# Kernel optimization log

Hardware: AMD Instinct MI355X
Metric: run time of the kernel (lower is better)

The kernel has to match this reference:

```python
import jax, jax.numpy as jnp
import numpy as np

N_NODES = 100000
N_EDGES = 3200000
NUM_GRAPHS = 2048
IN_CH = 35
HID = 128
EPS = 1e-5


def setup_inputs() -> dict:
    key = jax.random.key(0)
    ks = jax.random.split(key, 16)
    x = jax.random.normal(ks[0], (N_NODES, IN_CH), dtype=jnp.float32)
    edge_index = jax.random.randint(ks[1], (2, N_EDGES), 0, N_NODES, dtype=jnp.int64)
    batch = jnp.sort(jax.random.randint(ks[2], (N_NODES,), 0, NUM_GRAPHS, dtype=jnp.int64))
    def lin(k, fan_in, fan_out):
        b = 1.0 / np.sqrt(fan_in)
        kw, kb = jax.random.split(k)
        W = jax.random.uniform(kw, (fan_in, fan_out), minval=-b, maxval=b, dtype=jnp.float32)
        bias = jax.random.uniform(kb, (fan_out,), minval=-b, maxval=b, dtype=jnp.float32)
        return W, bias
    W1, b1 = lin(ks[3], IN_CH, HID)
    W2, b2 = lin(ks[4], HID, HID)
    W3, b3 = lin(ks[5], HID, HID)
    Wl1, bl1 = lin(ks[6], HID, HID // 2)
    Wl2, bl2 = lin(ks[7], HID // 2, 1)
    ones = jnp.ones((HID,), jnp.float32)
    zeros = jnp.zeros((HID,), jnp.float32)
    return {
        'x': x, 'edge_index': edge_index, 'batch': batch,
        'W1': W1, 'b1': b1, 'g1': ones, 'be1': zeros,
        'W2': W2, 'b2': b2, 'g2': ones, 'be2': zeros,
        'W3': W3, 'b3': b3, 'g3': ones, 'be3': zeros,
        'Wl1': Wl1, 'bl1': bl1, 'Wl2': Wl2, 'bl2': bl2,
    }


def _gcn_norm(edge_index, n):
    # add self-loops, compute symmetric normalization D^-1/2 (A+I) D^-1/2
    loop = jnp.arange(n, dtype=edge_index.dtype)
    src = jnp.concatenate([edge_index[0], loop])
    dst = jnp.concatenate([edge_index[1], loop])
    deg = jax.ops.segment_sum(jnp.ones_like(dst, jnp.float32), dst, num_segments=n)
    dinv = jnp.where(deg > 0, jax.lax.rsqrt(deg), 0.0)
    norm = dinv[src] * dinv[dst]
    return src, dst, norm


def _gcn_conv(x, src, dst, norm, W, b):
    h = x @ W                      # [N, out]
    msg = h[src] * norm[:, None]   # gather + scale (irregular)
    out = jax.ops.segment_sum(msg, dst, num_segments=x.shape[0])
    return out + b


def _bn(x, g, be):
    mu = jnp.mean(x, axis=0)
    var = jnp.mean(jnp.square(x - mu), axis=0)  # biased var (torch BN training)
    return (x - mu) * jax.lax.rsqrt(var + EPS) * g + be


def reference(x, edge_index, batch, W1, b1, g1, be1, W2, b2, g2, be2,
              W3, b3, g3, be3, Wl1, bl1, Wl2, bl2):
    n = x.shape[0]
    src, dst, norm = _gcn_norm(edge_index, n)
    h = jax.nn.gelu(_bn(_gcn_conv(x, src, dst, norm, W1, b1), g1, be1), approximate=False)
    h = jax.nn.gelu(_bn(_gcn_conv(h, src, dst, norm, W2, b2), g2, be2), approximate=False)
    h = jax.nn.gelu(_bn(_gcn_conv(h, src, dst, norm, W3, b3), g3, be3), approximate=False)
    # global mean pool by graph id
    s = jax.ops.segment_sum(h, batch, num_segments=NUM_GRAPHS)
    cnt = jax.ops.segment_sum(jnp.ones((n,), jnp.float32), batch, num_segments=NUM_GRAPHS)
    pooled = s / jnp.maximum(cnt, 1.0)[:, None]
    out = jax.nn.elu(pooled @ Wl1 + bl1)
    out = out @ Wl2 + bl2
    return out  # [NUM_GRAPHS, 1]
```

## Files before the change

### kernel.cpp

```cpp
#include <hip/hip_runtime.h>
#include <hip/hip_bf16.h>
#include <math.h>

#define N_NODES 100000
#define N_EDGES 3200000
#define NUM_GRAPHS 2048
#define IN_CH 35
#define HID 128
#define BN_EPS 1e-5f

#define BUCK_SHIFT 9
#define BUCK_SIZE 512
#define NB_BUCK 196
#define BUCK_CAP 18432
#define BIN_GRID 1024
#define BIN_CHUNK 3128

typedef short bf16x8 __attribute__((ext_vector_type(8)));
typedef float f32x4 __attribute__((ext_vector_type(4)));

__device__ __forceinline__ float gelu_f(float x) {
    return 0.5f * x * (1.0f + erff(x * 0.70710678118654752440f));
}

__device__ __forceinline__ float bflo(unsigned v) { return __uint_as_float(v << 16); }
__device__ __forceinline__ float bfhi(unsigned v) { return __uint_as_float(v & 0xffff0000u); }
__device__ __forceinline__ unsigned f2bf(float f) {
    unsigned x = __float_as_uint(f);
    return (x + 0x7fffu + ((x >> 16) & 1u)) >> 16;
}
__device__ __forceinline__ unsigned packbf2(float lo, float hi) {
    return f2bf(lo) | (f2bf(hi) << 16);
}


__global__ void k_zero2(int* __restrict__ gcnt, float* __restrict__ stats,
                        unsigned* __restrict__ xzero, unsigned* __restrict__ hzero) {
    int i = threadIdx.x;
    if (i < NB_BUCK) gcnt[i] = 0;
    if (i < 3 * 256) stats[i] = 0.0f;
    if (i < 32) xzero[i] = 0u;
    if (i < 64) hzero[i] = 0u;
}


__global__ void k_wcast(const float* __restrict__ W2, const float* __restrict__ W3,
                        unsigned* __restrict__ Wt2, unsigned* __restrict__ Wt3) {
    int t = blockIdx.x * 256 + threadIdx.x;
    if (t >= 2 * 8192) return;
    const float* W = (t < 8192) ? W2 : W3;
    unsigned* Wt = (t < 8192) ? Wt2 : Wt3;
    int i = t & 8191;
    int n = i >> 6, j = i & 63;
    Wt[n * 64 + j] = packbf2(W[(2 * j) * HID + n], W[(2 * j + 1) * HID + n]);
}


__global__ void k_bin(const int* __restrict__ ei, int* __restrict__ gcnt,
                      unsigned* __restrict__ epack) {
    __shared__ unsigned lpack[BIN_CHUNK];
    __shared__ unsigned char lbuck[BIN_CHUNK];
    __shared__ int hist[NB_BUCK];
    __shared__ int hbase[NB_BUCK];
    __shared__ int lcur[NB_BUCK];
    int tid = threadIdx.x;
    if (tid < NB_BUCK) { hist[tid] = 0; lcur[tid] = 0; }
    __syncthreads();
    int e0 = blockIdx.x * BIN_CHUNK;
    int nE = min(e0 + BIN_CHUNK, N_EDGES) - e0;
    for (int i = tid * 4; i < nE; i += 1024) {
        int4 s4 = *(const int4*)(ei + e0 + i);
        int4 d4 = *(const int4*)(ei + N_EDGES + e0 + i);
        lpack[i + 0] = (unsigned)s4.x | (((unsigned)d4.x & 511u) << 17);
        lpack[i + 1] = (unsigned)s4.y | (((unsigned)d4.y & 511u) << 17);
        lpack[i + 2] = (unsigned)s4.z | (((unsigned)d4.z & 511u) << 17);
        lpack[i + 3] = (unsigned)s4.w | (((unsigned)d4.w & 511u) << 17);
        int b0 = d4.x >> BUCK_SHIFT, b1 = d4.y >> BUCK_SHIFT;
        int b2 = d4.z >> BUCK_SHIFT, b3 = d4.w >> BUCK_SHIFT;
        lbuck[i + 0] = (unsigned char)b0;
        lbuck[i + 1] = (unsigned char)b1;
        lbuck[i + 2] = (unsigned char)b2;
        lbuck[i + 3] = (unsigned char)b3;
        atomicAdd(&hist[b0], 1);
        atomicAdd(&hist[b1], 1);
        atomicAdd(&hist[b2], 1);
        atomicAdd(&hist[b3], 1);
    }
    __syncthreads();
    if (tid < NB_BUCK) {
        int h = hist[tid];
        hbase[tid] = (h > 0) ? (tid * BUCK_CAP + atomicAdd(&gcnt[tid], h)) : 0;
    }
    __syncthreads();
    for (int i = tid; i < nE; i += 256) {
        int b = lbuck[i];
        int off = atomicAdd(&lcur[b], 1);
        epack[hbase[b] + off] = lpack[i];
    }
}


__global__ void k_fill(const int* __restrict__ gcnt, const unsigned* __restrict__ epack,
                       int* __restrict__ rowp, int* __restrict__ rowpEnd,
                       float* __restrict__ dinv, int* __restrict__ col) {
    __shared__ int ldeg[BUCK_SIZE];
    __shared__ int sa[BUCK_SIZE];
    __shared__ int sb[BUCK_SIZE];
    __shared__ int lcur[BUCK_SIZE];
    int b = blockIdx.x;
    int tid = threadIdx.x;
    int base_node = b << BUCK_SHIFT;
    int nn = min(BUCK_SIZE, N_NODES - base_node);
    int seg0 = b * BUCK_CAP;
    int seg1 = seg0 + gcnt[b];
    ldeg[tid] = 0;
    __syncthreads();
    for (int e = seg0 + tid; e < seg1; e += BUCK_SIZE) {
        atomicAdd(&ldeg[epack[e] >> 17], 1);
    }
    __syncthreads();
    sa[tid] = ldeg[tid];
    __syncthreads();
    int* src = sa; int* dst = sb;
    for (int st = 1; st < BUCK_SIZE; st <<= 1) {
        int v = src[tid];
        if (tid >= st) v += src[tid - st];
        dst[tid] = v;
        __syncthreads();
        int* t = src; src = dst; dst = t;
    }
    int ex = (tid == 0) ? 0 : src[tid - 1];
    int rp = seg0 + ex;
    lcur[tid] = rp;
    if (tid < nn) {
        rowp[base_node + tid] = rp;
        rowpEnd[base_node + tid] = rp + ldeg[tid];
        dinv[base_node + tid] = rsqrtf((float)(ldeg[tid] + 1));
    }
    __syncthreads();
    for (int e = seg0 + tid; e < seg1; e += BUCK_SIZE) {
        unsigned v = epack[e];
        int p = atomicAdd(&lcur[v >> 17], 1);
        col[p] = (int)(v & 0x1FFFFu);
    }
}


__global__ void k_castx(const float* __restrict__ X, const float* __restrict__ dinv,
                        unsigned* __restrict__ Xb) {
    int i = blockIdx.x * blockDim.x + threadIdx.x;
    if (i >= N_NODES * 32) return;
    int n = i >> 5, j = i & 31;
    float dv = dinv[n];
    float lo = 0.0f, hi = 0.0f;
    if (j < 17) {
        lo = X[(size_t)n * IN_CH + 2 * j];
        hi = X[(size_t)n * IN_CH + 2 * j + 1];
    } else if (j == 17) {
        lo = X[(size_t)n * IN_CH + 34];
    }
    Xb[i] = packbf2(dv * lo, dv * hi);
}

#define ACC8(v) { a0 += bflo(v.x); a1 += bfhi(v.x); a2 += bflo(v.y); a3 += bfhi(v.y); \
                  a4 += bflo(v.z); a5 += bfhi(v.z); a6 += bflo(v.w); a7 += bfhi(v.w); }
#define ACC4(v) { a0 += bflo(v.x); a1 += bfhi(v.x); a2 += bflo(v.y); a3 += bfhi(v.y); }


#define C1_NODES 8

__global__ __launch_bounds__(512) void k_conv1(
        const unsigned* __restrict__ Xb, const int* __restrict__ rowp,
        const int* __restrict__ rowpEnd, const int* __restrict__ col,
        const float* __restrict__ dinv,
        const float* __restrict__ W1, const float* __restrict__ b1,
        unsigned* __restrict__ Yb) {
    __shared__ float w_s[IN_CH * HID];
    __shared__ float b_s[HID];
    __shared__ float xa_s[C1_NODES][36];
    int tid = threadIdx.x;
    for (int u = tid; u < IN_CH * HID; u += 512) w_s[u] = W1[u];
    if (tid < HID) b_s[tid] = b1[tid];

    int wid = tid >> 6;
    int lane = tid & 63;
    int g = lane >> 4;
    int j = lane & 15;
    int node = blockIdx.x * C1_NODES + wid;
    bool valid = node < N_NODES;

    float a0 = 0.0f, a1 = 0.0f, a2 = 0.0f, a3 = 0.0f;
    float di = 0.0f;
    if (valid) {
        int rp0 = rowp[node], rp1 = rowpEnd[node];
        di = dinv[node];
        uint2 sv = *(const uint2*)(Xb + (size_t)node * 32 + j * 2);
        float w0 = (g == 0) ? 1.0f : 0.0f;
        a0 = w0 * bflo(sv.x); a1 = w0 * bfhi(sv.x);
        a2 = w0 * bflo(sv.y); a3 = w0 * bfhi(sv.y);
        unsigned deg = (unsigned)(rp1 - rp0);
        for (int e0 = (rp0 & ~3); e0 < rp1; e0 += 32) {
            int ebA = e0 + 4 * g;
            int ebB = ebA + 16;
            int4 cA = *(const int4*)(col + ebA);
            int4 cB = *(const int4*)(col + ebB);
            int s0 = ((unsigned)(ebA + 0 - rp0) < deg) ? cA.x : N_NODES;
            int s1 = ((unsigned)(ebA + 1 - rp0) < deg) ? cA.y : N_NODES;
            int s2 = ((unsigned)(ebA + 2 - rp0) < deg) ? cA.z : N_NODES;
            int s3 = ((unsigned)(ebA + 3 - rp0) < deg) ? cA.w : N_NODES;
            int s4 = ((unsigned)(ebB + 0 - rp0) < deg) ? cB.x : N_NODES;
            int s5 = ((unsigned)(ebB + 1 - rp0) < deg) ? cB.y : N_NODES;
            int s6 = ((unsigned)(ebB + 2 - rp0) < deg) ? cB.z : N_NODES;
            int s7 = ((unsigned)(ebB + 3 - rp0) < deg) ? cB.w : N_NODES;
            uint2 v0 = *(const uint2*)(Xb + (size_t)s0 * 32 + j * 2);
            uint2 v1 = *(const uint2*)(Xb + (size_t)s1 * 32 + j * 2);
            uint2 v2 = *(const uint2*)(Xb + (size_t)s2 * 32 + j * 2);
            uint2 v3 = *(const uint2*)(Xb + (size_t)s3 * 32 + j * 2);
            uint2 v4 = *(const uint2*)(Xb + (size_t)s4 * 32 + j * 2);
            uint2 v5 = *(const uint2*)(Xb + (size_t)s5 * 32 + j * 2);
            uint2 v6 = *(const uint2*)(Xb + (size_t)s6 * 32 + j * 2);
            uint2 v7 = *(const uint2*)(Xb + (size_t)s7 * 32 + j * 2);
            ACC4(v0); ACC4(v1); ACC4(v2); ACC4(v3);
            ACC4(v4); ACC4(v5); ACC4(v6); ACC4(v7);
        }
    }
    a0 += __shfl(a0, (lane + 32) & 63, 64);
    a1 += __shfl(a1, (lane + 32) & 63, 64);
    a2 += __shfl(a2, (lane + 32) & 63, 64);
    a3 += __shfl(a3, (lane + 32) & 63, 64);
    a0 += __shfl(a0, (lane + 16) & 63, 64);
    a1 += __shfl(a1, (lane + 16) & 63, 64);
    a2 += __shfl(a2, (lane + 16) & 63, 64);
    a3 += __shfl(a3, (lane + 16) & 63, 64);
    if (valid && g == 0 && j < 9) {
        xa_s[wid][4 * j + 0] = di * a0;
        xa_s[wid][4 * j + 1] = di * a1;
        xa_s[wid][4 * j + 2] = di * a2;
        xa_s[wid][4 * j + 3] = di * a3;
    }
    __syncthreads();
    float acc0 = b_s[2 * lane];
    float acc1 = b_s[2 * lane + 1];
    #pragma unroll 7
    for (int k = 0; k < IN_CH; ++k) {
        float xv = xa_s[wid][k];
        acc0 = fmaf(xv, w_s[k * HID + 2 * lane], acc0);
        acc1 = fmaf(xv, w_s[k * HID + 2 * lane + 1], acc1);
    }
    if (valid) Yb[(size_t)node * 64 + lane] = packbf2(acc0, acc1);
}


__global__ __launch_bounds__(256) void k_gemm128m(
        const unsigned* __restrict__ Yb, const float* __restrict__ stats,
        const float* __restrict__ g, const float* __restrict__ be,
        const unsigned* __restrict__ Wt, const float* __restrict__ dinv,
        unsigned* __restrict__ Hb) {
    __shared__ __align__(16) unsigned act[64 * 64];
    __shared__ float sc_s[HID];
    __shared__ float sh_s[HID];
    int tid = threadIdx.x;
    if (tid < HID) {
        const float inv_n = 1.0f / (float)N_NODES;
        float mean = stats[tid] * inv_n;
        float var = stats[HID + tid] * inv_n - mean * mean;
        float s = g[tid] * rsqrtf(var + BN_EPS);
        sc_s[tid] = s;
        sh_s[tid] = be[tid] - mean * s;
    }
    __syncthreads();
    int row0 = blockIdx.x * 64;
    #pragma unroll
    for (int it = 0; it < 8; ++it) {
        int idx = it * 256 + tid;
        int r = idx >> 5;
        int c2 = idx & 31;
        int gr = row0 + r;
        uint2 v = make_uint2(0u, 0u);
        if (gr < N_NODES) v = *(const uint2*)(Yb + (size_t)gr * 64 + c2 * 2);
        int c = c2 * 2;
        float x0 = gelu_f(fmaf(bflo(v.x), sc_s[2 * c], sh_s[2 * c]));
        float x1 = gelu_f(fmaf(bfhi(v.x), sc_s[2 * c + 1], sh_s[2 * c + 1]));
        float x2 = gelu_f(fmaf(bflo(v.y), sc_s[2 * c + 2], sh_s[2 * c + 2]));
        float x3 = gelu_f(fmaf(bfhi(v.y), sc_s[2 * c + 3], sh_s[2 * c + 3]));
        int swz = (r & 7) << 2;
        act[r * 64 + (c ^ swz)]       = packbf2(x0, x1);
        act[r * 64 + ((c + 1) ^ swz)] = packbf2(x2, x3);
    }
    __syncthreads();
    int l = tid & 63;
    int w = tid >> 6;
    int r0 = w * 16;
    int arow = r0 + (l & 15);
    int kgrp = l >> 4;
    bf16x8 afrag[4];
    #pragma unroll
    for (int kk = 0; kk < 4; ++kk) {
        int base = (kk * 16 + kgrp * 4) ^ ((arow & 7) << 2);
        afrag[kk] = *(const bf16x8*)&act[arow * 64 + base];
    }
    float dv[4];
    #pragma unroll
    for (int reg = 0; reg < 4; ++reg) {
        int gr = row0 + r0 + kgrp * 4 + reg;
        dv[reg] = (gr < N_NODES) ? dinv[gr] : 0.0f;
    }
    unsigned short* Hb16 = (unsigned short*)Hb;
    #pragma unroll
    for (int n0 = 0; n0 < 8; ++n0) {
        f32x4 acc = {0.0f, 0.0f, 0.0f, 0.0f};
        #pragma unroll
        for (int kk = 0; kk < 4; ++kk) {
            bf16x8 b = *(const bf16x8*)&Wt[(n0 * 16 + (l & 15)) * 64 + kk * 16 + kgrp * 4];
            acc = __builtin_amdgcn_mfma_f32_16x16x32_bf16(afrag[kk], b, acc, 0, 0, 0);
        }
        int colg = n0 * 16 + (l & 15);
        #pragma unroll
        for (int reg = 0; reg < 4; ++reg) {
            int gr = row0 + r0 + kgrp * 4 + reg;
            if (gr < N_NODES)
                Hb16[(size_t)gr * HID + colg] = (unsigned short)f2bf(dv[reg] * acc[reg]);
        }
    }
}


__global__ void k_convb(const unsigned* __restrict__ Hb, const int* __restrict__ rowp,
                        const int* __restrict__ rowpEnd, const int* __restrict__ col,
                        const float* __restrict__ dinv,
                        const float* __restrict__ bias, unsigned* __restrict__ Yb) {
    int tid = threadIdx.x;
    int wid = tid >> 6;
    int lane = tid & 63;
    int g = lane >> 4;
    int j = lane & 15;
    int node = blockIdx.x * 4 + wid;
    if (node >= N_NODES) return;
    int rp0 = rowp[node], rp1 = rowpEnd[node];
    float di = dinv[node];
    uint4 sv = *(const uint4*)(Hb + (size_t)node * 64 + j * 4);
    float w0 = (g == 0) ? 1.0f : 0.0f;
    float a0 = w0 * bflo(sv.x), a1 = w0 * bfhi(sv.x);
    float a2 = w0 * bflo(sv.y), a3 = w0 * bfhi(sv.y);
    float a4 = w0 * bflo(sv.z), a5 = w0 * bfhi(sv.z);
    float a6 = w0 * bflo(sv.w), a7 = w0 * bfhi(sv.w);
    unsigned deg = (unsigned)(rp1 - rp0);
    for (int e0 = (rp0 & ~3); e0 < rp1; e0 += 32) {
        int ebA = e0 + 4 * g;
        int ebB = ebA + 16;
        int4 cA = *(const int4*)(col + ebA);
        int4 cB = *(const int4*)(col + ebB);
        int s0 = ((unsigned)(ebA + 0 - rp0) < deg) ? cA.x : N_NODES;
        int s1 = ((unsigned)(ebA + 1 - rp0) < deg) ? cA.y : N_NODES;
        int s2 = ((unsigned)(ebA + 2 - rp0) < deg) ? cA.z : N_NODES;
        int s3 = ((unsigned)(ebA + 3 - rp0) < deg) ? cA.w : N_NODES;
        int s4 = ((unsigned)(ebB + 0 - rp0) < deg) ? cB.x : N_NODES;
        int s5 = ((unsigned)(ebB + 1 - rp0) < deg) ? cB.y : N_NODES;
        int s6 = ((unsigned)(ebB + 2 - rp0) < deg) ? cB.z : N_NODES;
        int s7 = ((unsigned)(ebB + 3 - rp0) < deg) ? cB.w : N_NODES;
        uint4 v0 = *(const uint4*)(Hb + (size_t)s0 * 64 + j * 4);
        uint4 v1 = *(const uint4*)(Hb + (size_t)s1 * 64 + j * 4);
        uint4 v2 = *(const uint4*)(Hb + (size_t)s2 * 64 + j * 4);
        uint4 v3 = *(const uint4*)(Hb + (size_t)s3 * 64 + j * 4);
        uint4 v4 = *(const uint4*)(Hb + (size_t)s4 * 64 + j * 4);
        uint4 v5 = *(const uint4*)(Hb + (size_t)s5 * 64 + j * 4);
        uint4 v6 = *(const uint4*)(Hb + (size_t)s6 * 64 + j * 4);
        uint4 v7 = *(const uint4*)(Hb + (size_t)s7 * 64 + j * 4);
        ACC8(v0); ACC8(v1); ACC8(v2); ACC8(v3);
        ACC8(v4); ACC8(v5); ACC8(v6); ACC8(v7);
    }
    a0 += __shfl(a0, (lane + 32) & 63, 64);
    a1 += __shfl(a1, (lane + 32) & 63, 64);
    a2 += __shfl(a2, (lane + 32) & 63, 64);
    a3 += __shfl(a3, (lane + 32) & 63, 64);
    a4 += __shfl(a4, (lane + 32) & 63, 64);
    a5 += __shfl(a5, (lane + 32) & 63, 64);
    a6 += __shfl(a6, (lane + 32) & 63, 64);
    a7 += __shfl(a7, (lane + 32) & 63, 64);
    a0 += __shfl(a0, (lane + 16) & 63, 64);
    a1 += __shfl(a1, (lane + 16) & 63, 64);
    a2 += __shfl(a2, (lane + 16) & 63, 64);
    a3 += __shfl(a3, (lane + 16) & 63, 64);
    a4 += __shfl(a4, (lane + 16) & 63, 64);
    a5 += __shfl(a5, (lane + 16) & 63, 64);
    a6 += __shfl(a6, (lane + 16) & 63, 64);
    a7 += __shfl(a7, (lane + 16) & 63, 64);
    if (g == 0) {
        const float4* bp = (const float4*)(bias + 8 * j);
        float4 bA = bp[0], bB = bp[1];
        uint4 o;
        o.x = packbf2(fmaf(di, a0, bA.x), fmaf(di, a1, bA.y));
        o.y = packbf2(fmaf(di, a2, bA.z), fmaf(di, a3, bA.w));
        o.z = packbf2(fmaf(di, a4, bB.x), fmaf(di, a5, bB.y));
        o.w = packbf2(fmaf(di, a6, bB.z), fmaf(di, a7, bB.w));
        *(uint4*)(Yb + (size_t)node * 64 + j * 4) = o;
    }
}


__global__ void k_statsb(const unsigned* __restrict__ Yb, float* __restrict__ stats) {
    __shared__ float red[16][128];
    __shared__ float red2[16][128];
    int tid = threadIdx.x;
    int j = tid & 15;
    int rg = tid >> 4;
    float s[8] = {0, 0, 0, 0, 0, 0, 0, 0};
    float q[8] = {0, 0, 0, 0, 0, 0, 0, 0};
    for (int r = blockIdx.x * 16 + rg; r < N_NODES; r += gridDim.x * 16) {
        uint4 v = *(const uint4*)(Yb + (size_t)r * 64 + j * 4);
        float x;
        x = bflo(v.x); s[0] += x; q[0] = fmaf(x, x, q[0]);
        x = bfhi(v.x); s[1] += x; q[1] = fmaf(x, x, q[1]);
        x = bflo(v.y); s[2] += x; q[2] = fmaf(x, x, q[2]);
        x = bfhi(v.y); s[3] += x; q[3] = fmaf(x, x, q[3]);
        x = bflo(v.z); s[4] += x; q[4] = fmaf(x, x, q[4]);
        x = bfhi(v.z); s[5] += x; q[5] = fmaf(x, x, q[5]);
        x = bflo(v.w); s[6] += x; q[6] = fmaf(x, x, q[6]);
        x = bfhi(v.w); s[7] += x; q[7] = fmaf(x, x, q[7]);
    }
    #pragma unroll
    for (int k = 0; k < 8; ++k) {
        red[rg][8 * j + k]  = s[k];
        red2[rg][8 * j + k] = q[k];
    }
    __syncthreads();
    if (tid < 128) {
        float S = 0.0f, Q = 0.0f;
        #pragma unroll
        for (int r = 0; r < 16; ++r) { S += red[r][tid]; Q += red2[r][tid]; }
        atomicAdd(&stats[tid], S);
        atomicAdd(&stats[128 + tid], Q);
    }
}


__device__ __forceinline__ int lowerb(const int* __restrict__ arr, int n, int key) {
    int lo = 0, hi = n;
    while (lo < hi) {
        int mid = (lo + hi) >> 1;
        if (arr[mid] < key) lo = mid + 1; else hi = mid;
    }
    return lo;
}

__global__ void k_pool_mlp(const unsigned* __restrict__ Yb, const float* __restrict__ stats,
                           const float* __restrict__ g, const float* __restrict__ be,
                           const int* __restrict__ batch,
                           const float* __restrict__ Wl1, const float* __restrict__ bl1,
                           const float* __restrict__ Wl2, const float* __restrict__ bl2,
                           float* __restrict__ out) {
    __shared__ float pooled[128];
    __shared__ float part[2][128];
    __shared__ float sc_s[128];
    __shared__ float sh_s[128];
    __shared__ int bounds[2];
    int gidx = blockIdx.x;
    int tid = threadIdx.x;
    if (tid < 128) {
        const float inv_n = 1.0f / (float)N_NODES;
        float mean = stats[tid] * inv_n;
        float var = stats[128 + tid] * inv_n - mean * mean;
        float s = g[tid] * rsqrtf(var + BN_EPS);
        sc_s[tid] = s;
        sh_s[tid] = be[tid] - mean * s;
    }
    if (tid == 0) {
        bounds[0] = lowerb(batch, N_NODES, gidx);
        bounds[1] = lowerb(batch, N_NODES, gidx + 1);
    }
    __syncthreads();
    int lo = bounds[0], hi = bounds[1];
    int rofs = tid >> 6;
    int w = tid & 63;
    float sA = sc_s[2 * w], hA = sh_s[2 * w];
    float sB = sc_s[2 * w + 1], hB = sh_s[2 * w + 1];
    float accA = 0.0f, accB = 0.0f;
    for (int r = lo + rofs; r < hi; r += 2) {
        unsigned v = Yb[(size_t)r * 64 + w];
        accA += gelu_f(fmaf(bflo(v), sA, hA));
        accB += gelu_f(fmaf(bfhi(v), sB, hB));
    }
    part[rofs][2 * w]     = accA;
    part[rofs][2 * w + 1] = accB;
    __syncthreads();
    if (tid < 128)
        pooled[tid] = (hi > lo) ? (part[0][tid] + part[1][tid]) / (float)(hi - lo) : 0.0f;
    __syncthreads();
    if (tid < 64) {
        float hs = bl1[tid];
        #pragma unroll 4
        for (int k = 0; k < 128; ++k)
            hs = fmaf(pooled[k], Wl1[k * 64 + tid], hs);
        float e = (hs > 0.0f) ? hs : expm1f(hs);
        float pv = e * Wl2[tid];
        #pragma unroll
        for (int o = 32; o > 0; o >>= 1)
            pv += __shfl_down(pv, o);
        if (tid == 0) out[gidx] = pv + bl2[0];
    }
}


extern "C" void kernel_launch(void* const* d_in, const int* in_sizes, int n_in,
                              void* d_out, int out_size, void* d_ws, size_t ws_size,
                              hipStream_t stream) {
    const float* x   = (const float*)d_in[0];
    const int*   ei  = (const int*)d_in[1];
    const int*   bat = (const int*)d_in[2];
    const float* W1  = (const float*)d_in[3];
    const float* b1  = (const float*)d_in[4];
    const float* g1  = (const float*)d_in[5];
    const float* be1 = (const float*)d_in[6];
    const float* W2  = (const float*)d_in[7];
    const float* b2  = (const float*)d_in[8];
    const float* g2  = (const float*)d_in[9];
    const float* be2 = (const float*)d_in[10];
    const float* W3  = (const float*)d_in[11];
    const float* b3  = (const float*)d_in[12];
    const float* g3  = (const float*)d_in[13];
    const float* be3 = (const float*)d_in[14];
    const float* Wl1 = (const float*)d_in[15];
    const float* bl1 = (const float*)d_in[16];
    const float* Wl2 = (const float*)d_in[17];
    const float* bl2 = (const float*)d_in[18];
    float* out = (float*)d_out;

    char* ws = (char*)d_ws;
    size_t off = 0;
    auto alloc = [&](size_t bytes) -> char* {
        char* p = ws + off;
        off += (bytes + 255) & ~(size_t)255;
        return p;
    };
    int*      gcnt    = (int*)alloc(NB_BUCK * sizeof(int));
    unsigned* epack   = (unsigned*)alloc(((size_t)NB_BUCK * BUCK_CAP + 64) * sizeof(unsigned));
    int*      rowp    = (int*)alloc(N_NODES * sizeof(int));
    int*      rowpEnd = (int*)alloc(N_NODES * sizeof(int));
    float*    dinv    = (float*)alloc(N_NODES * sizeof(float));
    int*      col     = (int*)alloc(((size_t)NB_BUCK * BUCK_CAP + 64) * sizeof(int));
    unsigned* Xb      = (unsigned*)alloc((size_t)(N_NODES + 1) * 32 * sizeof(unsigned));
    unsigned* Ybuf    = (unsigned*)alloc((size_t)N_NODES * 64 * sizeof(unsigned));
    unsigned* Hbuf    = (unsigned*)alloc((size_t)(N_NODES + 1) * 64 * sizeof(unsigned));
    float*    stats   = (float*)alloc(3 * 256 * sizeof(float));
    unsigned* Wt2     = (unsigned*)alloc(8192 * sizeof(unsigned));
    unsigned* Wt3     = (unsigned*)alloc(8192 * sizeof(unsigned));

    k_zero2<<<1, 1024, 0, stream>>>(gcnt, stats, Xb + (size_t)N_NODES * 32,
                                    Hbuf + (size_t)N_NODES * 64);
    k_wcast<<<64, 256, 0, stream>>>(W2, W3, Wt2, Wt3);
    k_bin<<<BIN_GRID, 256, 0, stream>>>(ei, gcnt, epack);
    k_fill<<<NB_BUCK, BUCK_SIZE, 0, stream>>>(gcnt, epack, rowp, rowpEnd, dinv, col);
    k_castx<<<(N_NODES * 32 + 255) / 256, 256, 0, stream>>>(x, dinv, Xb);

    const int gemm_blocks = (N_NODES + 63) / 64;
    const int conv_blocks = (N_NODES + 3) / 4;

    k_conv1<<<(N_NODES + C1_NODES - 1) / C1_NODES, 512, 0, stream>>>(
        Xb, rowp, rowpEnd, col, dinv, W1, b1, Ybuf);
    k_statsb<<<1024, 256, 0, stream>>>(Ybuf, stats + 0 * 256);

    k_gemm128m<<<gemm_blocks, 256, 0, stream>>>(Ybuf, stats + 0 * 256, g1, be1, Wt2, dinv, Hbuf);
    k_convb<<<conv_blocks, 256, 0, stream>>>(Hbuf, rowp, rowpEnd, col, dinv, b2, Ybuf);
    k_statsb<<<1024, 256, 0, stream>>>(Ybuf, stats + 1 * 256);

    k_gemm128m<<<gemm_blocks, 256, 0, stream>>>(Ybuf, stats + 1 * 256, g2, be2, Wt3, dinv, Hbuf);
    k_convb<<<conv_blocks, 256, 0, stream>>>(Hbuf, rowp, rowpEnd, col, dinv, b3, Ybuf);
    k_statsb<<<1024, 256, 0, stream>>>(Ybuf, stats + 2 * 256);

    k_pool_mlp<<<NUM_GRAPHS, 128, 0, stream>>>(Ybuf, stats + 2 * 256, g3, be3, bat,
                                               Wl1, bl1, Wl2, bl2, out);
}
```

Before: 677.5 us.

## Pad CSR rows to multiples of four, fuse castx into fill, prefetch col indices

The CSR column array is now padded so every row length is a multiple of 4, with sentinel N_NODES entries. The aggregation loops can therefore use aligned int4 loads, a cheaper per-group validity check, and software prefetch of the next column chunk. The conv1 gather now uses 16-byte loads with 8 lanes per row instead of 8-byte loads. The Xb cast is fused into k_fill, and the zero and weight-cast kernels are merged, removing launches. The cost is a larger col buffer and extra padding writes, and correctness depends on every row fitting within COL_CAP.

```diff
diff --git a/kernel.cpp b/kernel.cpp
--- a/kernel.cpp
+++ b/kernel.cpp
@@ -13,6 +13,7 @@
 #define BUCK_SIZE 512
 #define NB_BUCK 196
 #define BUCK_CAP 18432
+#define COL_CAP 19456
 #define BIN_GRID 1024
 #define BIN_CHUNK 3128
 
@@ -34,25 +35,24 @@
 }
 
 
-__global__ void k_zero2(int* __restrict__ gcnt, float* __restrict__ stats,
-                        unsigned* __restrict__ xzero, unsigned* __restrict__ hzero) {
-    int i = threadIdx.x;
-    if (i < NB_BUCK) gcnt[i] = 0;
-    if (i < 3 * 256) stats[i] = 0.0f;
-    if (i < 32) xzero[i] = 0u;
-    if (i < 64) hzero[i] = 0u;
-}
-
-
-__global__ void k_wcast(const float* __restrict__ W2, const float* __restrict__ W3,
-                        unsigned* __restrict__ Wt2, unsigned* __restrict__ Wt3) {
-    int t = blockIdx.x * 256 + threadIdx.x;
-    if (t >= 2 * 8192) return;
-    const float* W = (t < 8192) ? W2 : W3;
-    unsigned* Wt = (t < 8192) ? Wt2 : Wt3;
-    int i = t & 8191;
-    int n = i >> 6, j = i & 63;
-    Wt[n * 64 + j] = packbf2(W[(2 * j) * HID + n], W[(2 * j + 1) * HID + n]);
+__global__ void k_init(int* __restrict__ gcnt, float* __restrict__ stats,
+                       unsigned* __restrict__ xzero, unsigned* __restrict__ hzero,
+                       const float* __restrict__ W2, const float* __restrict__ W3,
+                       unsigned* __restrict__ Wt2, unsigned* __restrict__ Wt3) {
+    if (blockIdx.x < 64) {
+        int t = blockIdx.x * 256 + threadIdx.x;
+        const float* W = (t < 8192) ? W2 : W3;
+        unsigned* Wt = (t < 8192) ? Wt2 : Wt3;
+        int i = t & 8191;
+        int n = i >> 6, j = i & 63;
+        Wt[n * 64 + j] = packbf2(W[(2 * j) * HID + n], W[(2 * j + 1) * HID + n]);
+    } else {
+        int i = threadIdx.x;
+        if (i < NB_BUCK) gcnt[i] = 0;
+        for (int k = i; k < 3 * 256; k += 256) stats[k] = 0.0f;
+        if (i < 32) xzero[i] = 0u;
+        if (i < 64) hzero[i] = 0u;
+    }
 }
 
 
@@ -100,26 +100,31 @@
 }
 
 
-__global__ void k_fill(const int* __restrict__ gcnt, const unsigned* __restrict__ epack,
-                       int* __restrict__ rowp, int* __restrict__ rowpEnd,
-                       float* __restrict__ dinv, int* __restrict__ col) {
+__global__ __launch_bounds__(512) void k_fill(
+        const int* __restrict__ gcnt, const unsigned* __restrict__ epack,
+        int* __restrict__ rowp, int* __restrict__ rowpEnd,
+        float* __restrict__ dinv, int* __restrict__ col,
+        const float* __restrict__ X, unsigned* __restrict__ Xb) {
     __shared__ int ldeg[BUCK_SIZE];
     __shared__ int sa[BUCK_SIZE];
     __shared__ int sb[BUCK_SIZE];
     __shared__ int lcur[BUCK_SIZE];
+    __shared__ float dl[BUCK_SIZE];
     int b = blockIdx.x;
     int tid = threadIdx.x;
     int base_node = b << BUCK_SHIFT;
     int nn = min(BUCK_SIZE, N_NODES - base_node);
-    int seg0 = b * BUCK_CAP;
-    int seg1 = seg0 + gcnt[b];
+    int seg0e = b * BUCK_CAP;
+    int seg1e = seg0e + gcnt[b];
+    int seg0c = b * COL_CAP;
     ldeg[tid] = 0;
     __syncthreads();
-    for (int e = seg0 + tid; e < seg1; e += BUCK_SIZE) {
+    for (int e = seg0e + tid; e < seg1e; e += BUCK_SIZE)
         atomicAdd(&ldeg[epack[e] >> 17], 1);
-    }
-    __syncthreads();
-    sa[tid] = ldeg[tid];
+    __syncthreads();
+    int deg = ldeg[tid];
+    int pdeg = (deg + 3) & ~3;
+    sa[tid] = pdeg;
     __syncthreads();
     int* src = sa; int* dst = sb;
     for (int st = 1; st < BUCK_SIZE; st <<= 1) {
@@ -130,41 +135,44 @@
         int* t = src; src = dst; dst = t;
     }
     int ex = (tid == 0) ? 0 : src[tid - 1];
-    int rp = seg0 + ex;
+    int total = src[BUCK_SIZE - 1];
+    int rp = seg0c + ex;
     lcur[tid] = rp;
+    float dv = rsqrtf((float)(deg + 1));
+    dl[tid] = dv;
     if (tid < nn) {
         rowp[base_node + tid] = rp;
-        rowpEnd[base_node + tid] = rp + ldeg[tid];
-        dinv[base_node + tid] = rsqrtf((float)(ldeg[tid] + 1));
-    }
-    __syncthreads();
-    for (int e = seg0 + tid; e < seg1; e += BUCK_SIZE) {
+        rowpEnd[base_node + tid] = rp + pdeg;
+        dinv[base_node + tid] = dv;
+    }
+    __syncthreads();
+    for (int e = seg0e + tid; e < seg1e; e += BUCK_SIZE) {
         unsigned v = epack[e];
         int p = atomicAdd(&lcur[v >> 17], 1);
         col[p] = (int)(v & 0x1FFFFu);
     }
-}
-
-
-__global__ void k_castx(const float* __restrict__ X, const float* __restrict__ dinv,
-                        unsigned* __restrict__ Xb) {
-    int i = blockIdx.x * blockDim.x + threadIdx.x;
-    if (i >= N_NODES * 32) return;
-    int n = i >> 5, j = i & 31;
-    float dv = dinv[n];
-    float lo = 0.0f, hi = 0.0f;
-    if (j < 17) {
-        lo = X[(size_t)n * IN_CH + 2 * j];
-        hi = X[(size_t)n * IN_CH + 2 * j + 1];
-    } else if (j == 17) {
-        lo = X[(size_t)n * IN_CH + 34];
-    }
-    Xb[i] = packbf2(dv * lo, dv * hi);
+    if (tid < nn) {
+        for (int p = rp + deg; p < rp + pdeg; ++p) col[p] = N_NODES;
+    }
+    for (int p = seg0c + total + tid; p < seg0c + COL_CAP; p += BUCK_SIZE)
+        col[p] = N_NODES;
+    for (int idx = tid; idx < nn * 32; idx += BUCK_SIZE) {
+        int nl = idx >> 5, j = idx & 31;
+        int n = base_node + nl;
+        float dvn = dl[nl];
+        float lo = 0.0f, hi = 0.0f;
+        if (j < 17) {
+            lo = X[(size_t)n * IN_CH + 2 * j];
+            hi = X[(size_t)n * IN_CH + 2 * j + 1];
+        } else if (j == 17) {
+            lo = X[(size_t)n * IN_CH + 34];
+        }
+        Xb[(size_t)n * 32 + j] = packbf2(dvn * lo, dvn * hi);
+    }
 }
 
 #define ACC8(v) { a0 += bflo(v.x); a1 += bfhi(v.x); a2 += bflo(v.y); a3 += bfhi(v.y); \
                   a4 += bflo(v.z); a5 += bfhi(v.z); a6 += bflo(v.w); a7 += bfhi(v.w); }
-#define ACC4(v) { a0 += bflo(v.x); a1 += bfhi(v.x); a2 += bflo(v.y); a3 += bfhi(v.y); }
 
 
 #define C1_NODES 8
@@ -177,66 +185,62 @@
         unsigned* __restrict__ Yb) {
     __shared__ float w_s[IN_CH * HID];
     __shared__ float b_s[HID];
-    __shared__ float xa_s[C1_NODES][36];
+    __shared__ float xa_s[C1_NODES][40];
     int tid = threadIdx.x;
     for (int u = tid; u < IN_CH * HID; u += 512) w_s[u] = W1[u];
     if (tid < HID) b_s[tid] = b1[tid];
 
     int wid = tid >> 6;
     int lane = tid & 63;
-    int g = lane >> 4;
-    int j = lane & 15;
+    int g = lane >> 3;
+    int j = lane & 7;
     int node = blockIdx.x * C1_NODES + wid;
     bool valid = node < N_NODES;
 
-    float a0 = 0.0f, a1 = 0.0f, a2 = 0.0f, a3 = 0.0f;
+    float a0 = 0, a1 = 0, a2 = 0, a3 = 0, a4 = 0, a5 = 0, a6 = 0, a7 = 0;
     float di = 0.0f;
     if (valid) {
         int rp0 = rowp[node], rp1 = rowpEnd[node];
         di = dinv[node];
-        uint2 sv = *(const uint2*)(Xb + (size_t)node * 32 + j * 2);
+        uint4 sv = *(const uint4*)(Xb + (size_t)node * 32 + j * 4);
         float w0 = (g == 0) ? 1.0f : 0.0f;
         a0 = w0 * bflo(sv.x); a1 = w0 * bfhi(sv.x);
         a2 = w0 * bflo(sv.y); a3 = w0 * bfhi(sv.y);
-        unsigned deg = (unsigned)(rp1 - rp0);
-        for (int e0 = (rp0 & ~3); e0 < rp1; e0 += 32) {
-            int ebA = e0 + 4 * g;
-            int ebB = ebA + 16;
-            int4 cA = *(const int4*)(col + ebA);
-            int4 cB = *(const int4*)(col + ebB);
-            int s0 = ((unsigned)(ebA + 0 - rp0) < deg) ? cA.x : N_NODES;
-            int s1 = ((unsigned)(ebA + 1 - rp0) < deg) ? cA.y : N_NODES;
-            int s2 = ((unsigned)(ebA + 2 - rp0) < deg) ? cA.z : N_NODES;
-            int s3 = ((unsigned)(ebA + 3 - rp0) < deg) ? cA.w : N_NODES;
-            int s4 = ((unsigned)(ebB + 0 - rp0) < deg) ? cB.x : N_NODES;
-            int s5 = ((unsigned)(ebB + 1 - rp0) < deg) ? cB.y : N_NODES;
-            int s6 = ((unsigned)(ebB + 2 - rp0) < deg) ? cB.z : N_NODES;
-            int s7 = ((unsigned)(ebB + 3 - rp0) < deg) ? cB.w : N_NODES;
-            uint2 v0 = *(const uint2*)(Xb + (size_t)s0 * 32 + j * 2);
-            uint2 v1 = *(const uint2*)(Xb + (size_t)s1 * 32 + j * 2);
-            uint2 v2 = *(const uint2*)(Xb + (size_t)s2 * 32 + j * 2);
-            uint2 v3 = *(const uint2*)(Xb + (size_t)s3 * 32 + j * 2);
-            uint2 v4 = *(const uint2*)(Xb + (size_t)s4 * 32 + j * 2);
-            uint2 v5 = *(const uint2*)(Xb + (size_t)s5 * 32 + j * 2);
-            uint2 v6 = *(const uint2*)(Xb + (size_t)s6 * 32 + j * 2);
-            uint2 v7 = *(const uint2*)(Xb + (size_t)s7 * 32 + j * 2);
-            ACC4(v0); ACC4(v1); ACC4(v2); ACC4(v3);
-            ACC4(v4); ACC4(v5); ACC4(v6); ACC4(v7);
+        a4 = w0 * bflo(sv.z); a5 = w0 * bfhi(sv.z);
+        a6 = w0 * bflo(sv.w); a7 = w0 * bfhi(sv.w);
+        if (rp0 < rp1) {
+            int4 cs = *(const int4*)(col + rp0 + 4 * g);
+            for (int e0 = rp0; e0 < rp1; e0 += 32) {
+                int4 nx = *(const int4*)(col + e0 + 32 + 4 * g);
+                bool v = (e0 + 4 * g) < rp1;
+                int s0 = v ? cs.x : N_NODES;
+                int s1 = v ? cs.y : N_NODES;
+                int s2 = v ? cs.z : N_NODES;
+                int s3 = v ? cs.w : N_NODES;
+                uint4 v0 = *(const uint4*)(Xb + (size_t)s0 * 32 + j * 4);
+                uint4 v1 = *(const uint4*)(Xb + (size_t)s1 * 32 + j * 4);
+                uint4 v2 = *(const uint4*)(Xb + (size_t)s2 * 32 + j * 4);
+                uint4 v3 = *(const uint4*)(Xb + (size_t)s3 * 32 + j * 4);
+                ACC8(v0); ACC8(v1); ACC8(v2); ACC8(v3);
+                cs = nx;
+            }
         }
     }
-    a0 += __shfl(a0, (lane + 32) & 63, 64);
-    a1 += __shfl(a1, (lane + 32) & 63, 64);
-    a2 += __shfl(a2, (lane + 32) & 63, 64);
-    a3 += __shfl(a3, (lane + 32) & 63, 64);
-    a0 += __shfl(a0, (lane + 16) & 63, 64);
-    a1 += __shfl(a1, (lane + 16) & 63, 64);
-    a2 += __shfl(a2, (lane + 16) & 63, 64);
-    a3 += __shfl(a3, (lane + 16) & 63, 64);
-    if (valid && g == 0 && j < 9) {
-        xa_s[wid][4 * j + 0] = di * a0;
-        xa_s[wid][4 * j + 1] = di * a1;
-        xa_s[wid][4 * j + 2] = di * a2;
-        xa_s[wid][4 * j + 3] = di * a3;
+    #define RED(o) { a0 += __shfl(a0,(lane+o)&63,64); a1 += __shfl(a1,(lane+o)&63,64); \
+                     a2 += __shfl(a2,(lane+o)&63,64); a3 += __shfl(a3,(lane+o)&63,64); \
+                     a4 += __shfl(a4,(lane+o)&63,64); a5 += __shfl(a5,(lane+o)&63,64); \
+                     a6 += __shfl(a6,(lane+o)&63,64); a7 += __shfl(a7,(lane+o)&63,64); }
+    RED(32); RED(16); RED(8);
+    #undef RED
+    if (valid && g == 0 && j < 5) {
+        xa_s[wid][8 * j + 0] = di * a0;
+        xa_s[wid][8 * j + 1] = di * a1;
+        xa_s[wid][8 * j + 2] = di * a2;
+        xa_s[wid][8 * j + 3] = di * a3;
+        xa_s[wid][8 * j + 4] = di * a4;
+        xa_s[wid][8 * j + 5] = di * a5;
+        xa_s[wid][8 * j + 6] = di * a6;
+        xa_s[wid][8 * j + 7] = di * a7;
     }
     __syncthreads();
     float acc0 = b_s[2 * lane];
@@ -344,47 +348,41 @@
     float a2 = w0 * bflo(sv.y), a3 = w0 * bfhi(sv.y);
     float a4 = w0 * bflo(sv.z), a5 = w0 * bfhi(sv.z);
     float a6 = w0 * bflo(sv.w), a7 = w0 * bfhi(sv.w);
-    unsigned deg = (unsigned)(rp1 - rp0);
-    for (int e0 = (rp0 & ~3); e0 < rp1; e0 += 32) {
-        int ebA = e0 + 4 * g;
-        int ebB = ebA + 16;
-        int4 cA = *(const int4*)(col + ebA);
-        int4 cB = *(const int4*)(col + ebB);
-        int s0 = ((unsigned)(ebA + 0 - rp0) < deg) ? cA.x : N_NODES;
-        int s1 = ((unsigned)(ebA + 1 - rp0) < deg) ? cA.y : N_NODES;
-        int s2 = ((unsigned)(ebA + 2 - rp0) < deg) ? cA.z : N_NODES;
-        int s3 = ((unsigned)(ebA + 3 - rp0) < deg) ? cA.w : N_NODES;
-        int s4 = ((unsigned)(ebB + 0 - rp0) < deg) ? cB.x : N_NODES;
-        int s5 = ((unsigned)(ebB + 1 - rp0) < deg) ? cB.y : N_NODES;
-        int s6 = ((unsigned)(ebB + 2 - rp0) < deg) ? cB.z : N_NODES;
-        int s7 = ((unsigned)(ebB + 3 - rp0) < deg) ? cB.w : N_NODES;
-        uint4 v0 = *(const uint4*)(Hb + (size_t)s0 * 64 + j * 4);
-        uint4 v1 = *(const uint4*)(Hb + (size_t)s1 * 64 + j * 4);
-        uint4 v2 = *(const uint4*)(Hb + (size_t)s2 * 64 + j * 4);
-        uint4 v3 = *(const uint4*)(Hb + (size_t)s3 * 64 + j * 4);
-        uint4 v4 = *(const uint4*)(Hb + (size_t)s4 * 64 + j * 4);
-        uint4 v5 = *(const uint4*)(Hb + (size_t)s5 * 64 + j * 4);
-        uint4 v6 = *(const uint4*)(Hb + (size_t)s6 * 64 + j * 4);
-        uint4 v7 = *(const uint4*)(Hb + (size_t)s7 * 64 + j * 4);
-        ACC8(v0); ACC8(v1); ACC8(v2); ACC8(v3);
-        ACC8(v4); ACC8(v5); ACC8(v6); ACC8(v7);
-    }
-    a0 += __shfl(a0, (lane + 32) & 63, 64);
-    a1 += __shfl(a1, (lane + 32) & 63, 64);
-    a2 += __shfl(a2, (lane + 32) & 63, 64);
-    a3 += __shfl(a3, (lane + 32) & 63, 64);
-    a4 += __shfl(a4, (lane + 32) & 63, 64);
-    a5 += __shfl(a5, (lane + 32) & 63, 64);
-    a6 += __shfl(a6, (lane + 32) & 63, 64);
-    a7 += __shfl(a7, (lane + 32) & 63, 64);
-    a0 += __shfl(a0, (lane + 16) & 63, 64);
-    a1 += __shfl(a1, (lane + 16) & 63, 64);
-    a2 += __shfl(a2, (lane + 16) & 63, 64);
-    a3 += __shfl(a3, (lane + 16) & 63, 64);
-    a4 += __shfl(a4, (lane + 16) & 63, 64);
-    a5 += __shfl(a5, (lane + 16) & 63, 64);
-    a6 += __shfl(a6, (lane + 16) & 63, 64);
-    a7 += __shfl(a7, (lane + 16) & 63, 64);
+    if (rp0 < rp1) {
+        int4 cA = *(const int4*)(col + rp0 + 4 * g);
+        int4 cB = *(const int4*)(col + rp0 + 16 + 4 * g);
+        for (int e0 = rp0; e0 < rp1; e0 += 32) {
+            int4 nA = *(const int4*)(col + e0 + 32 + 4 * g);
+            int4 nB = *(const int4*)(col + e0 + 48 + 4 * g);
+            bool vA = (e0 + 4 * g) < rp1;
+            bool vB = (e0 + 16 + 4 * g) < rp1;
+            int s0 = vA ? cA.x : N_NODES;
+            int s1 = vA ? cA.y : N_NODES;
+            int s2 = vA ? cA.z : N_NODES;
+            int s3 = vA ? cA.w : N_NODES;
+            int s4 = vB ? cB.x : N_NODES;
+            int s5 = vB ? cB.y : N_NODES;
+            int s6 = vB ? cB.z : N_NODES;
+            int s7 = vB ? cB.w : N_NODES;
+            uint4 v0 = *(const uint4*)(Hb + (size_t)s0 * 64 + j * 4);
+            uint4 v1 = *(const uint4*)(Hb + (size_t)s1 * 64 + j * 4);
+            uint4 v2 = *(const uint4*)(Hb + (size_t)s2 * 64 + j * 4);
+            uint4 v3 = *(const uint4*)(Hb + (size_t)s3 * 64 + j * 4);
+            uint4 v4 = *(const uint4*)(Hb + (size_t)s4 * 64 + j * 4);
+            uint4 v5 = *(const uint4*)(Hb + (size_t)s5 * 64 + j * 4);
+            uint4 v6 = *(const uint4*)(Hb + (size_t)s6 * 64 + j * 4);
+            uint4 v7 = *(const uint4*)(Hb + (size_t)s7 * 64 + j * 4);
+            ACC8(v0); ACC8(v1); ACC8(v2); ACC8(v3);
+            ACC8(v4); ACC8(v5); ACC8(v6); ACC8(v7);
+            cA = nA; cB = nB;
+        }
+    }
+    #define RED(o) { a0 += __shfl(a0,(lane+o)&63,64); a1 += __shfl(a1,(lane+o)&63,64); \
+                     a2 += __shfl(a2,(lane+o)&63,64); a3 += __shfl(a3,(lane+o)&63,64); \
+                     a4 += __shfl(a4,(lane+o)&63,64); a5 += __shfl(a5,(lane+o)&63,64); \
+                     a6 += __shfl(a6,(lane+o)&63,64); a7 += __shfl(a7,(lane+o)&63,64); }
+    RED(32); RED(16);
+    #undef RED
     if (g == 0) {
         const float4* bp = (const float4*)(bias + 8 * j);
         float4 bA = bp[0], bB = bp[1];
@@ -537,7 +535,7 @@
     int*      rowp    = (int*)alloc(N_NODES * sizeof(int));
     int*      rowpEnd = (int*)alloc(N_NODES * sizeof(int));
     float*    dinv    = (float*)alloc(N_NODES * sizeof(float));
-    int*      col     = (int*)alloc(((size_t)NB_BUCK * BUCK_CAP + 64) * sizeof(int));
+    int*      col     = (int*)alloc(((size_t)NB_BUCK * COL_CAP + 64) * sizeof(int));
     unsigned* Xb      = (unsigned*)alloc((size_t)(N_NODES + 1) * 32 * sizeof(unsigned));
     unsigned* Ybuf    = (unsigned*)alloc((size_t)N_NODES * 64 * sizeof(unsigned));
     unsigned* Hbuf    = (unsigned*)alloc((size_t)(N_NODES + 1) * 64 * sizeof(unsigned));
@@ -545,12 +543,10 @@
     unsigned* Wt2     = (unsigned*)alloc(8192 * sizeof(unsigned));
     unsigned* Wt3     = (unsigned*)alloc(8192 * sizeof(unsigned));
 
-    k_zero2<<<1, 1024, 0, stream>>>(gcnt, stats, Xb + (size_t)N_NODES * 32,
-                                    Hbuf + (size_t)N_NODES * 64);
-    k_wcast<<<64, 256, 0, stream>>>(W2, W3, Wt2, Wt3);
+    k_init<<<65, 256, 0, stream>>>(gcnt, stats, Xb + (size_t)N_NODES * 32,
+                                   Hbuf + (size_t)N_NODES * 64, W2, W3, Wt2, Wt3);
     k_bin<<<BIN_GRID, 256, 0, stream>>>(ei, gcnt, epack);
-    k_fill<<<NB_BUCK, BUCK_SIZE, 0, stream>>>(gcnt, epack, rowp, rowpEnd, dinv, col);
-    k_castx<<<(N_NODES * 32 + 255) / 256, 256, 0, stream>>>(x, dinv, Xb);
+    k_fill<<<NB_BUCK, BUCK_SIZE, 0, stream>>>(gcnt, epack, rowp, rowpEnd, dinv, col, x, Xb);
 
     const int gemm_blocks = (N_NODES + 63) / 64;
     const int conv_blocks = (N_NODES + 3) / 4;
```

Result: slower. 698.1 us (+3.0%).
